# Performance work log

Hardware: AMD Instinct MI355X
Metric: run time of the kernel (lower is better)

## Reference

```python
import jax, jax.numpy as jnp
import numpy as np

B, C, H, W = 4, 64, 64, 64
CI = C // 2  # inter_channels


def setup_inputs() -> dict:
    key = jax.random.key(0)
    k1, k2, k3, k4, k5 = jax.random.split(key, 5)
    x = jax.random.normal(k1, (B, C, H, W), dtype=jnp.float32)
    # 1x1 conv g: in C -> CI (weight [CI, C], bias [CI])
    Wg = jax.random.normal(k2, (CI, C), dtype=jnp.float32) * (1.0 / np.sqrt(C))
    bg = jax.random.normal(k3, (CI,), dtype=jnp.float32) * 0.01
    # 1x1 conv W_z: CI -> C
    Wz = jax.random.normal(k4, (C, CI), dtype=jnp.float32) * (1.0 / np.sqrt(CI))
    bz = jax.random.normal(k5, (C,), dtype=jnp.float32) * 0.01
    return {"x": x, "Wg": Wg, "bg": bg, "Wz": Wz, "bz": bz}


def reference(x, Wg, bg, Wz, bz):
    b, c, h, w = x.shape
    n = h * w
    xf = x.reshape(b, c, n)                       # [B,C,N]
    # g projection (1x1 conv) then flatten: [B,N,CI]
    g_x = jnp.einsum('bcn,oc->bno', xf, Wg) + bg  # [B,N,CI]
    # theta = phi = raw x flattened
    theta = xf.transpose(0, 2, 1)                 # [B,N,C]
    f = jnp.einsum('bnc,bcm->bnm', theta, xf)     # [B,N,N]
    f_div_C = jax.nn.softmax(f, axis=-1)
    y = jnp.einsum('bnm,bmo->bno', f_div_C, g_x)  # [B,N,CI]
    y = y.transpose(0, 2, 1).reshape(b, CI, h, w)  # [B,CI,H,W]
    # W_z projection (1x1 conv) + residual
    W_y = jnp.einsum('oi,bihw->bohw', Wz, y) + bz[None, :, None, None]
    return W_y + x
```

## Files before the change

kernel.cpp:

```cpp
#include <hip/hip_runtime.h>
#include <hip/hip_bf16.h>
#include <math.h>

#define B_  4
#define C_  64
#define N_  4096
#define CI_ 32

typedef __attribute__((ext_vector_type(8))) unsigned short u16x8;
typedef __attribute__((ext_vector_type(8))) __bf16        bf16x8;
typedef __attribute__((ext_vector_type(4))) __bf16        bf16x4;
typedef __attribute__((ext_vector_type(4))) float         f32x4;

__device__ __forceinline__ unsigned short f2bf(float f) {
    union { float f; unsigned int i; } v; v.f = f;
    unsigned int r = v.i + 0x7FFFu + ((v.i >> 16) & 1u);
    return (unsigned short)(r >> 16);
}

__global__ __launch_bounds__(256) void k_prep(
    const float* __restrict__ x, const float* __restrict__ Wg,
    const float* __restrict__ bg, unsigned short* __restrict__ xT,
    unsigned short* __restrict__ gx, float* __restrict__ diag)
{
    __shared__ __align__(16) float tile[64][68];
    __shared__ float part[4][64][33];
    const int t  = threadIdx.x;
    const int b  = blockIdx.x >> 6;
    const int n0 = (blockIdx.x & 63) * 64;

    #pragma unroll
    for (int pass = 0; pass < 4; ++pass) {
        int c   = (t >> 4) + pass * 16;
        int nl4 = (t & 15) * 4;
        float4 v = *(const float4*)(x + (size_t)(b * C_ + c) * N_ + n0 + nl4);
        *(float4*)&tile[c][nl4] = v;
    }
    __syncthreads();

    {
        const int n  = t >> 2;
        const int cc = (t & 3) * 16;
        u16x8 a, b2;
        #pragma unroll
        for (int j = 0; j < 8; ++j) a[j]  = f2bf(tile[cc + j][n]);
        #pragma unroll
        for (int j = 0; j < 8; ++j) b2[j] = f2bf(tile[cc + 8 + j][n]);
        unsigned short* dst = xT + (size_t)(b * N_ + n0 + n) * C_ + cc;
        *(u16x8*)dst       = a;
        *(u16x8*)(dst + 8) = b2;
    }
    {
        const int nl = t & 63, cq = t >> 6;
        float acc[CI_];
        #pragma unroll
        for (int o = 0; o < CI_; ++o) acc[o] = 0.f;
        float dd = 0.f;
        #pragma unroll 4
        for (int cl = 0; cl < 16; ++cl) {
            int c = cq * 16 + cl;
            float xv = tile[c][nl];
            dd += xv * xv;
            #pragma unroll
            for (int o = 0; o < CI_; ++o) acc[o] += Wg[o * C_ + c] * xv;
        }
        #pragma unroll
        for (int o = 0; o < CI_; ++o) part[cq][nl][o] = acc[o];
        part[cq][nl][32] = dd;
    }
    __syncthreads();
    {
        const int o = t >> 3, nr = (t & 7) * 8;
        u16x8 w;
        #pragma unroll
        for (int j = 0; j < 8; ++j) {
            int n = nr + j;
            float s = part[0][n][o] + part[1][n][o] + part[2][n][o] + part[3][n][o]
                    + bg[o];
            w[j] = f2bf(s);
        }
        *(u16x8*)(gx + (size_t)(b * CI_ + o) * N_ + n0 + nr) = w;
    }
    if (t < 64)
        diag[(size_t)b * N_ + n0 + t] =
            part[0][t][32] + part[1][t][32] + part[2][t][32] + part[3][t][32];
}

__device__ __forceinline__ f32x4 mfma16(bf16x8 a, bf16x8 b, f32x4 c) {
    return __builtin_amdgcn_mfma_f32_16x16x32_bf16(a, b, c, 0, 0, 0);
}

#define KLOAD(kr, tT)                                                          \
    kr[0] = *(const u16x8*)(kSrc0 + (size_t)(tT) * (32 * C_));                 \
    kr[1] = *(const u16x8*)(kSrc1 + (size_t)(tT) * (32 * C_));

#define KSTORE(bufS, kr)                                                       \
    *(u16x8*)((bufS) + kDst0) = kr[0];                                         \
    *(u16x8*)((bufS) + kDst1) = kr[1];

#define VLOAD(vr, tT)                                                          \
    vr[0] = *(const bf16x8*)(bBase0 + (tT) * 32);                              \
    vr[1] = *(const bf16x8*)(bBase1 + (tT) * 32);

#define COMPUTE(ABUF, Vr)                                                      \
    {                                                                          \
        bf16x8 Af[2][2];                                                       \
        _Pragma("unroll")                                                      \
        for (int kt = 0; kt < 2; ++kt) {                                       \
            _Pragma("unroll")                                                  \
            for (int kc = 0; kc < 2; ++kc)                                     \
                Af[kt][kc] = *(const bf16x8*)((ABUF)                           \
                    + (g * 32 + kt * 16 + li) * 72 + kc * 32 + quad * 8);      \
        }                                                                      \
        f32x4 S[2][2];                                                         \
        _Pragma("unroll")                                                      \
        for (int kt = 0; kt < 2; ++kt) {                                       \
            _Pragma("unroll")                                                  \
            for (int qt = 0; qt < 2; ++qt) {                                   \
                f32x4 z = (f32x4){nKq[qt], nKq[qt], nKq[qt], nKq[qt]};         \
                z = mfma16(Af[kt][0], Qf[qt][0], z);                           \
                S[kt][qt] = mfma16(Af[kt][1], Qf[qt][1], z);                   \
            }                                                                  \
        }                                                                      \
        _Pragma("unroll")                                                      \
        for (int qt = 0; qt < 2; ++qt) {                                       \
            _Pragma("unroll")                                                  \
            for (int kt = 0; kt < 2; ++kt) {                                   \
                bf16x4 pb;                                                     \
                _Pragma("unroll")                                              \
                for (int r = 0; r < 4; ++r) {                                  \
                    float p = __expf(S[kt][qt][r]);                            \
                    lacc[qt] += p;                                             \
                    pb[r] = (__bf16)p;                                         \
                }                                                              \
                *(bf16x4*)(pW + qt * 640 + kt * 16) = pb;                      \
            }                                                                  \
        }                                                                      \
        bf16x8 Ap[2];                                                          \
        _Pragma("unroll")                                                      \
        for (int qt = 0; qt < 2; ++qt)                                         \
            Ap[qt] = *(const bf16x8*)(pR + qt * 640);                          \
        _Pragma("unroll")                                                      \
        for (int qt = 0; qt < 2; ++qt) {                                       \
            _Pragma("unroll")                                                  \
            for (int ot = 0; ot < 2; ++ot)                                     \
                Yf[qt][ot] = mfma16(Ap[qt], Vr[ot], Yf[qt][ot]);               \
        }                                                                      \
    }

__global__ __launch_bounds__(256, 4) void k_flash(
    const unsigned short* __restrict__ xT, const unsigned short* __restrict__ gx,
    const float* __restrict__ diag,
    float* __restrict__ ypart, float* __restrict__ lpart)
{
    __shared__ __align__(16) char smem[28672];
    unsigned short* xk0 = (unsigned short*)smem;
    unsigned short* xk1 = (unsigned short*)(smem + 9216);
    unsigned short* Pl  = (unsigned short*)(smem + 18432);

    const int tid  = threadIdx.x;
    const int wave = tid >> 6, lane = tid & 63;
    const int quad = lane >> 4, li = lane & 15;
    const int g = wave >> 1, qh = wave & 1;
    const int bi  = blockIdx.x;
    const int kq  = bi & 3;
    const int qtb = (bi >> 2) & 63;
    const int b   = bi >> 8;
    const int qw  = qtb * 64 + qh * 32;
    const int u   = tid & 127;

    const unsigned short* xb = xT + (size_t)b * N_ * C_;
    const unsigned short* gb = gx + (size_t)b * CI_ * N_;

    float nKq[2];
    #pragma unroll
    for (int qt = 0; qt < 2; ++qt)
        nKq[qt] = -diag[(size_t)b * N_ + qw + qt * 16 + li];

    bf16x8 Qf[2][2];
    #pragma unroll
    for (int qt = 0; qt < 2; ++qt)
        #pragma unroll
        for (int kc = 0; kc < 2; ++kc)
            Qf[qt][kc] = *(const bf16x8*)(xb + (size_t)(qw + qt * 16 + li) * C_
                                          + kc * 32 + quad * 8);

    f32x4 Yf[2][2];
    #pragma unroll
    for (int qt = 0; qt < 2; ++qt)
        #pragma unroll
        for (int ot = 0; ot < 2; ++ot)
            Yf[qt][ot] = (f32x4){0.f, 0.f, 0.f, 0.f};
    float lacc[2] = {0.f, 0.f};

    const int keybase = kq * 1024 + g * 512;
    const int gg = tid >> 7;
    const int sbase = kq * 1024 + gg * 512;

    const int cc0 = u * 2,      key0 = cc0 >> 3, cof0 = (cc0 & 7) * 8;
    const int cc1 = u * 2 + 1,  key1 = cc1 >> 3, cof1 = (cc1 & 7) * 8;
    const unsigned short* kSrc0 = xb + (size_t)(sbase + key0) * C_ + cof0;
    const unsigned short* kSrc1 = xb + (size_t)(sbase + key1) * C_ + cof1;
    const int kDst0 = (gg * 32 + key0) * 72 + cof0;
    const int kDst1 = (gg * 32 + key1) * 72 + cof1;

    const unsigned short* bBase0 = gb + (size_t)(li) * N_      + keybase + quad * 8;
    const unsigned short* bBase1 = gb + (size_t)(16 + li) * N_ + keybase + quad * 8;

    unsigned short*       pW = Pl + (wave * 32 + li) * 40 + quad * 4;
    const unsigned short* pR = Pl + (wave * 32 + li) * 40 + quad * 8;

    u16x8  kA[2], kB[2];
    bf16x8 vA[2], vB[2], vA2[2], vB2[2];
    KLOAD(kA, 0) VLOAD(vA, 0)
    KLOAD(kB, 1) VLOAD(vB, 1)
    KSTORE(xk0, kA)
    KLOAD(kA, 2)
    __syncthreads();

    #pragma unroll 1
    for (int t2 = 0; t2 < 8; ++t2) {
        const int te  = 2 * t2;
        const int nk0 = (te + 3 < 16) ? te + 3 : 15;
        const int nv0 = (te + 2 < 16) ? te + 2 : 15;
        const int nk1 = (te + 4 < 16) ? te + 4 : 15;
        const int nv1 = (te + 3 < 16) ? te + 3 : 15;
        KSTORE(xk1, kB)
        KLOAD(kB, nk0)
        VLOAD(vA2, nv0)
        COMPUTE(xk0, vA)
        __syncthreads();
        KSTORE(xk0, kA)
        KLOAD(kA, nk1)
        VLOAD(vB2, nv1)
        COMPUTE(xk1, vB)
        __syncthreads();
        vA[0] = vA2[0]; vA[1] = vA2[1];
        vB[0] = vB2[0]; vB[1] = vB2[1];
    }

    #pragma unroll
    for (int qt = 0; qt < 2; ++qt) {
        lacc[qt] += __shfl_xor(lacc[qt], 16, 64);
        lacc[qt] += __shfl_xor(lacc[qt], 32, 64);
    }

    float* ym = (float*)smem;

    #pragma unroll
    for (int qt = 0; qt < 2; ++qt) {
        #pragma unroll
        for (int ot = 0; ot < 2; ++ot)
            #pragma unroll
            for (int r = 0; r < 4; ++r)
                ym[(wave * 32 + qt * 16 + quad * 4 + r) * 34 + ot * 16 + li] = Yf[qt][ot][r];
        if (quad == 0)
            ym[(wave * 32 + qt * 16 + li) * 34 + 32] = lacc[qt];
    }
    __syncthreads();
    {
        const int q = tid >> 2, og = tid & 3;
        const int qh2 = q >> 5, ql = q & 31;
        const int w0 = qh2, w1 = 2 + qh2;
        const size_t pbase = (size_t)(b * 64 + qtb) * 4 + kq;
        float* yp = ypart + pbase * 2048 + q * 32;
        #pragma unroll
        for (int j = 0; j < 8; ++j) {
            int o = og * 8 + j;
            yp[o] = ym[(w0 * 32 + ql) * 34 + o] + ym[(w1 * 32 + ql) * 34 + o];
        }
        if (og == 0)
            lpart[pbase * 64 + q] = ym[(w0 * 32 + ql) * 34 + 32]
                                  + ym[(w1 * 32 + ql) * 34 + 32];
    }
}

__global__ __launch_bounds__(256) void k_merge(
    const float* __restrict__ ypart, const float* __restrict__ lpart,
    const float* __restrict__ x, const float* __restrict__ Wz,
    const float* __restrict__ bz, float* __restrict__ out)
{
    __shared__ float yfin[64][33];
    const int t   = threadIdx.x;
    const int b   = blockIdx.x >> 6;
    const int qtb = blockIdx.x & 63;
    const int q0  = qtb * 64;

    {
        const int q = t >> 2, og = t & 3;
        const size_t pb = (size_t)(b * 64 + qtb) * 4;
        float l = lpart[(pb + 0) * 64 + q] + lpart[(pb + 1) * 64 + q]
                + lpart[(pb + 2) * 64 + q] + lpart[(pb + 3) * 64 + q];
        float inv = 1.f / l;
        #pragma unroll
        for (int j = 0; j < 8; ++j) {
            int o = og * 8 + j;
            float acc = 0.f;
            #pragma unroll
            for (int kq = 0; kq < 4; ++kq)
                acc += ypart[(pb + kq) * 2048 + q * 32 + o];
            yfin[q][o] = acc * inv;
        }
    }
    __syncthreads();
    {
        const int q = t & 63, c0 = t >> 6;
        #pragma unroll
        for (int i = 0; i < 16; ++i) {
            int cout = c0 + i * 4;
            float acc = bz[cout];
            #pragma unroll
            for (int o = 0; o < CI_; ++o)
                acc += Wz[cout * CI_ + o] * yfin[q][o];
            size_t oidx = (size_t)(b * C_ + cout) * N_ + q0 + q;
            out[oidx] = acc + x[oidx];
        }
    }
}

extern "C" void kernel_launch(void* const* d_in, const int* in_sizes, int n_in,
                              void* d_out, int out_size, void* d_ws, size_t ws_size,
                              hipStream_t stream) {
    (void)in_sizes; (void)n_in; (void)out_size; (void)ws_size;
    const float* x  = (const float*)d_in[0];
    const float* Wg = (const float*)d_in[1];
    const float* bg = (const float*)d_in[2];
    const float* Wz = (const float*)d_in[3];
    const float* bz = (const float*)d_in[4];
    float* out = (float*)d_out;

    unsigned short* xT = (unsigned short*)d_ws;
    unsigned short* gx = (unsigned short*)((char*)d_ws + 2097152);
    float* diag  = (float*)((char*)d_ws + 3145728);
    float* ypart = (float*)((char*)d_ws + 3211264);
    float* lpart = (float*)((char*)d_ws + 11599872);

    hipLaunchKernelGGL(k_prep,  dim3(B_ * (N_ / 64)),    dim3(256), 0, stream, x, Wg, bg, xT, gx, diag);
    hipLaunchKernelGGL(k_flash, dim3(B_ * 64 * 4),       dim3(256), 0, stream, xT, gx, diag, ypart, lpart);
    hipLaunchKernelGGL(k_merge, dim3(B_ * 64),           dim3(256), 0, stream, ypart, lpart, x, Wz, bz, out);
}
```

Before: 117.0 us.

## Feed softmax probabilities to PV MFMA directly from registers via 16x16x16 bf16

Uses the accumulator layout of the QK^T MFMA output directly as the A operand of the 16x16x16 bf16_1k MFMA for the P·V product, which removes the LDS write/read round trip for P. The V operand loads are re-indexed into 4-element chunks to match. This drops one LDS buffer and its traffic, and frees shared memory that may allow higher occupancy. The cost is twice as many MFMA instructions of half the K depth, which may have lower throughput than the 16x16x32 form.

```diff
diff --git a/kernel.cpp b/kernel.cpp
--- a/kernel.cpp
+++ b/kernel.cpp
@@ -11,6 +11,7 @@
 typedef __attribute__((ext_vector_type(8))) __bf16        bf16x8;
 typedef __attribute__((ext_vector_type(4))) __bf16        bf16x4;
 typedef __attribute__((ext_vector_type(4))) float         f32x4;
+typedef __attribute__((ext_vector_type(4))) short         short4b;
 
 __device__ __forceinline__ unsigned short f2bf(float f) {
     union { float f; unsigned int i; } v; v.f = f;
@@ -90,6 +91,17 @@
     return __builtin_amdgcn_mfma_f32_16x16x32_bf16(a, b, c, 0, 0, 0);
 }
 
+__device__ __forceinline__ f32x4 mfma1k(short4b a, short4b b, f32x4 c) {
+#if __has_builtin(__builtin_amdgcn_mfma_f32_16x16x16bf16_1k)
+    return __builtin_amdgcn_mfma_f32_16x16x16bf16_1k(a, b, c, 0, 0, 0);
+#else
+    f32x4 d = c;
+    asm volatile("v_mfma_f32_16x16x16_bf16 %0, %1, %2, %0"
+                 : "+v"(d) : "v"(a), "v"(b));
+    return d;
+#endif
+}
+
 #define KLOAD(kr, tT)                                                          \
     kr[0] = *(const u16x8*)(kSrc0 + (size_t)(tT) * (32 * C_));                 \
     kr[1] = *(const u16x8*)(kSrc1 + (size_t)(tT) * (32 * C_));
@@ -99,8 +111,10 @@
     *(u16x8*)((bufS) + kDst1) = kr[1];
 
 #define VLOAD(vr, tT)                                                          \
-    vr[0] = *(const bf16x8*)(bBase0 + (tT) * 32);                              \
-    vr[1] = *(const bf16x8*)(bBase1 + (tT) * 32);
+    vr[0][0] = *(const short4b*)(vb00 + (tT) * 32);                            \
+    vr[0][1] = *(const short4b*)(vb01 + (tT) * 32);                            \
+    vr[1][0] = *(const short4b*)(vb10 + (tT) * 32);                            \
+    vr[1][1] = *(const short4b*)(vb11 + (tT) * 32);
 
 #define COMPUTE(ABUF, Vr)                                                      \
     {                                                                          \
@@ -122,6 +136,7 @@
                 S[kt][qt] = mfma16(Af[kt][1], Qf[qt][1], z);                   \
             }                                                                  \
         }                                                                      \
+        short4b Pa[2][2];                                                      \
         _Pragma("unroll")                                                      \
         for (int qt = 0; qt < 2; ++qt) {                                       \
             _Pragma("unroll")                                                  \
@@ -133,18 +148,16 @@
                     lacc[qt] += p;                                             \
                     pb[r] = (__bf16)p;                                         \
                 }                                                              \
-                *(bf16x4*)(pW + qt * 640 + kt * 16) = pb;                      \
+                Pa[kt][qt] = *(short4b*)&pb;                                   \
             }                                                                  \
         }                                                                      \
-        bf16x8 Ap[2];                                                          \
-        _Pragma("unroll")                                                      \
-        for (int qt = 0; qt < 2; ++qt)                                         \
-            Ap[qt] = *(const bf16x8*)(pR + qt * 640);                          \
         _Pragma("unroll")                                                      \
         for (int qt = 0; qt < 2; ++qt) {                                       \
             _Pragma("unroll")                                                  \
-            for (int ot = 0; ot < 2; ++ot)                                     \
-                Yf[qt][ot] = mfma16(Ap[qt], Vr[ot], Yf[qt][ot]);               \
+            for (int ot = 0; ot < 2; ++ot) {                                   \
+                Yf[qt][ot] = mfma1k(Pa[0][qt], Vr[0][ot], Yf[qt][ot]);         \
+                Yf[qt][ot] = mfma1k(Pa[1][qt], Vr[1][ot], Yf[qt][ot]);         \
+            }                                                                  \
         }                                                                      \
     }
 
@@ -153,10 +166,9 @@
     const float* __restrict__ diag,
     float* __restrict__ ypart, float* __restrict__ lpart)
 {
-    __shared__ __align__(16) char smem[28672];
+    __shared__ __align__(16) char smem[18432];
     unsigned short* xk0 = (unsigned short*)smem;
     unsigned short* xk1 = (unsigned short*)(smem + 9216);
-    unsigned short* Pl  = (unsigned short*)(smem + 18432);
 
     const int tid  = threadIdx.x;
     const int wave = tid >> 6, lane = tid & 63;
@@ -204,14 +216,13 @@
     const int kDst0 = (gg * 32 + key0) * 72 + cof0;
     const int kDst1 = (gg * 32 + key1) * 72 + cof1;
 
-    const unsigned short* bBase0 = gb + (size_t)(li) * N_      + keybase + quad * 8;
-    const unsigned short* bBase1 = gb + (size_t)(16 + li) * N_ + keybase + quad * 8;
-
-    unsigned short*       pW = Pl + (wave * 32 + li) * 40 + quad * 4;
-    const unsigned short* pR = Pl + (wave * 32 + li) * 40 + quad * 8;
-
-    u16x8  kA[2], kB[2];
-    bf16x8 vA[2], vB[2], vA2[2], vB2[2];
+    const unsigned short* vb00 = gb + (size_t)(li) * N_      + keybase + quad * 4;
+    const unsigned short* vb01 = gb + (size_t)(16 + li) * N_ + keybase + quad * 4;
+    const unsigned short* vb10 = vb00 + 16;
+    const unsigned short* vb11 = vb01 + 16;
+
+    u16x8   kA[2], kB[2];
+    short4b vA[2][2], vB[2][2], vA2[2][2], vB2[2][2];
     KLOAD(kA, 0) VLOAD(vA, 0)
     KLOAD(kB, 1) VLOAD(vB, 1)
     KSTORE(xk0, kA)
@@ -235,8 +246,13 @@
         VLOAD(vB2, nv1)
         COMPUTE(xk1, vB)
         __syncthreads();
-        vA[0] = vA2[0]; vA[1] = vA2[1];
-        vB[0] = vB2[0]; vB[1] = vB2[1];
+        #pragma unroll
+        for (int kt = 0; kt < 2; ++kt)
+            #pragma unroll
+            for (int ot = 0; ot < 2; ++ot) {
+                vA[kt][ot] = vA2[kt][ot];
+                vB[kt][ot] = vB2[kt][ot];
+            }
     }
 
     #pragma unroll
```

Result: slower. 139.9 us (+19.6%).
